# Performance work log

Hardware: AMD Instinct MI355X
Metric: run time of the kernel (lower is better)

## Reference

```python
import jax, jax.numpy as jnp
import numpy as np

N_NODES = 100000
N_EDGES = 1600000
F_IN = 65
HIDDEN = 128
N_CLASSES = 32
NEG_SLOPE = 0.2


def _gat_conv(x0, src, dst, W, a_src, a_dst, b):
    """Single-head GAT-style conv: gather over edges, segment softmax, scatter-add."""
    h = x0 @ W                                  # [N, C]
    s = h @ a_src                                # [N]
    d = h @ a_dst                                # [N]
    e = jax.nn.leaky_relu(s[src] + d[dst], NEG_SLOPE)   # [E]
    m = jax.ops.segment_max(e, dst, num_segments=N_NODES)
    m = jnp.where(jnp.isfinite(m), m, 0.0)
    ex = jnp.exp(e - m[dst])                     # [E]
    denom = jax.ops.segment_sum(ex, dst, num_segments=N_NODES)
    alpha = ex / (denom[dst] + 1e-16)            # [E]
    out = jax.ops.segment_sum(h[src] * alpha[:, None], dst, num_segments=N_NODES)
    return out + b                               # [N, C]


def setup_inputs() -> dict:
    key = jax.random.key(0)
    ks = jax.random.split(key, 12)
    sc_in = 1.0 / np.sqrt(F_IN)
    sc_h = 1.0 / np.sqrt(HIDDEN)
    return {
        "x": jax.random.normal(ks[0], (N_NODES, F_IN), dtype=jnp.float32),
        "edge_index": jax.random.randint(ks[1], (2, N_EDGES), 0, N_NODES, dtype=jnp.int64),
        "W_mlp": jax.random.normal(ks[2], (F_IN, HIDDEN), dtype=jnp.float32) * sc_in,
        "b_mlp": jnp.zeros((HIDDEN,), dtype=jnp.float32),
        "W1": jax.random.normal(ks[3], (HIDDEN, N_CLASSES), dtype=jnp.float32) * sc_h,
        "a1_src": jax.random.normal(ks[4], (N_CLASSES,), dtype=jnp.float32) * 0.1,
        "a1_dst": jax.random.normal(ks[5], (N_CLASSES,), dtype=jnp.float32) * 0.1,
        "b1": jnp.zeros((N_CLASSES,), dtype=jnp.float32),
        "W2": jax.random.normal(ks[6], (HIDDEN, N_CLASSES), dtype=jnp.float32) * sc_h,
        "a2_src": jax.random.normal(ks[7], (N_CLASSES,), dtype=jnp.float32) * 0.1,
        "a2_dst": jax.random.normal(ks[8], (N_CLASSES,), dtype=jnp.float32) * 0.1,
        "b2": jnp.zeros((N_CLASSES,), dtype=jnp.float32),
    }


def reference(x, edge_index, W_mlp, b_mlp, W1, a1_src, a1_dst, b1, W2, a2_src, a2_dst, b2):
    src, dst = edge_index[0], edge_index[1]
    x0 = jax.nn.relu(x @ W_mlp + b_mlp)                      # [N, H]
    x1 = jax.nn.relu(_gat_conv(x0, src, dst, W1, a1_src, a1_dst, b1))  # [N, C]
    # dropout is identity in eval mode
    x2 = _gat_conv(x0, src, dst, W2, a2_src, a2_dst, b2)     # [N, C]
    x3 = jnp.max(x0, axis=-1, keepdims=True)                 # [N, 1]
    lngal_out = jnp.concatenate((x1, x2, x3), axis=-1) + x   # [N, 2C+1] == [N, F]
    return jax.nn.log_softmax(lngal_out, axis=1)
```

## Files before the change

kernel.cpp:

```cpp
#include <hip/hip_runtime.h>
#include <hip/hip_bf16.h>

#define NN 100000
#define NE 1600000
#define FIN 65
#define HID 128
#define NC 32
#define OUTC 65
#define NBUCK 391
#define CHUNKS 400
#define CH 4000
#define ESTRIDE 5120
#define NODE_BLOCKS 1563

typedef __attribute__((ext_vector_type(8))) short s8v;
typedef __attribute__((ext_vector_type(4))) float f4v;
#define MFMA16(a, b, c) __builtin_amdgcn_mfma_f32_16x16x32_bf16(a, b, c, 0, 0, 0)

__device__ __forceinline__ float lrelu(float v){ return v > 0.f ? v : 0.2f * v; }
__device__ __forceinline__ short f2bs(float f){
  unsigned u = __float_as_uint(f);
  u += 0x7fffu + ((u >> 16) & 1u);
  return (short)(u >> 16);
}
__device__ __forceinline__ float bfu_lo(unsigned u){ return __uint_as_float(u << 16); }
__device__ __forceinline__ float bfu_hi(unsigned u){ return __uint_as_float(u & 0xffff0000u); }

__global__ __launch_bounds__(256) void k_prep(
    const float* __restrict__ Wmlp, const float* __restrict__ W1,
    const float* __restrict__ W2, short* __restrict__ wbg,
    int* __restrict__ bcursor)
{
  const int i = blockIdx.x * 256 + threadIdx.x;
  if (blockIdx.x == 0)
    for (int t = threadIdx.x; t < NBUCK; t += 256) bcursor[t] = 0;
  {
    const int j = i & 7, l = (i >> 3) & 63, nt = (i >> 9) & 7, t = i >> 12;
    const int k = t * 32 + ((l >> 4) << 3) + j;
    const int col = (nt << 4) + (l & 15);
    wbg[i] = f2bs(Wmlp[k * HID + col]);
  }
  {
    const int j = i & 7, l = (i >> 3) & 63, nt = (i >> 9) & 3, t = i >> 11;
    const int k = t * 32 + ((l >> 4) << 3) + j;
    const int col = (nt << 4) + (l & 15);
    wbg[8192 + i] = f2bs(col < NC ? W1[k * NC + col] : W2[k * NC + col - NC]);
  }
}

__global__ __launch_bounds__(256) void k_main(
    const float* __restrict__ x, const short* __restrict__ wbg,
    const float* __restrict__ Wmlp, const float* __restrict__ bmlp,
    const float* __restrict__ a1s, const float* __restrict__ a1d,
    const float* __restrict__ a2s, const float* __restrict__ a2d,
    const int* __restrict__ ei,
    unsigned short* __restrict__ hb16,
    float* __restrict__ sd2, float* __restrict__ dd2,
    float* __restrict__ out,
    int* __restrict__ bcursor, int* __restrict__ ebuf)
{
  __shared__ alignas(16) char smem[28416];
  const int tid = threadIdx.x;

  if (blockIdx.x >= NODE_BLOCKS) {
    const int cb = blockIdx.x - NODE_BLOCKS;
    int* lh = (int*)smem;
    int* lbase = lh + NBUCK;
    for (int i = tid; i < NBUCK; i += 256) lh[i] = 0;
    __syncthreads();
    const int4* s4 = (const int4*)ei + cb * (CH / 4);
    const int4* d4 = (const int4*)(ei + NE) + cb * (CH / 4);
    for (int i = tid; i < CH / 4; i += 256) {
      int4 v = d4[i];
      atomicAdd(&lh[v.x >> 8], 1);
      atomicAdd(&lh[v.y >> 8], 1);
      atomicAdd(&lh[v.z >> 8], 1);
      atomicAdd(&lh[v.w >> 8], 1);
    }
    __syncthreads();
    for (int i = tid; i < NBUCK; i += 256) {
      int c = lh[i];
      lbase[i] = c ? (i * ESTRIDE + atomicAdd(&bcursor[i], c)) : 0;
      lh[i] = 0;
    }
    __syncthreads();
    for (int i = tid; i < CH / 4; i += 256) {
      int4 sv = s4[i];
      int4 dv = d4[i];
      int b, r;
      b = dv.x >> 8; r = atomicAdd(&lh[b], 1); ebuf[lbase[b] + r] = (sv.x << 8) | (dv.x & 255);
      b = dv.y >> 8; r = atomicAdd(&lh[b], 1); ebuf[lbase[b] + r] = (sv.y << 8) | (dv.y & 255);
      b = dv.z >> 8; r = atomicAdd(&lh[b], 1); ebuf[lbase[b] + r] = (sv.z << 8) | (dv.z & 255);
      b = dv.w >> 8; r = atomicAdd(&lh[b], 1); ebuf[lbase[b] + r] = (sv.w << 8) | (dv.w & 255);
    }
    return;
  }

  short* xbf = (short*)smem;
  short* x0b = (short*)(smem + 9216);
  float* xc64 = (float*)(smem + 26624);
  float* w64 = (float*)(smem + 26880);
  float* bmv = (float*)(smem + 27392);
  float* avv = (float*)(smem + 27904);

  const int base = blockIdx.x * 64;

  if (tid < 128) { w64[tid] = Wmlp[64 * HID + tid]; bmv[tid] = bmlp[tid]; }
  else if (tid < 160) {
    const int q = tid - 128;
    avv[q] = a1s[q]; avv[32 + q] = a1d[q]; avv[64 + q] = a2s[q]; avv[96 + q] = a2d[q];
  }
  for (int i = tid; i < 64 * 65; i += 256) {
    const int r = i / 65, c = i - r * 65;
    const int node = base + r;
    const float v = (node < NN) ? x[(size_t)node * FIN + c] : 0.f;
    if (c == 64) xc64[r] = v; else xbf[r * 72 + c] = f2bs(v);
  }
  __syncthreads();

  const int w = tid >> 6, lane = tid & 63;
  const int g = lane >> 4, q = lane & 15;
  const int rowA = w * 16 + q;
  const int rowD0 = w * 16 + g * 4;
  const s8v* wv8 = (const s8v*)wbg;

  const s8v a0 = *(const s8v*)&xbf[rowA * 72 + g * 8];
  const s8v a1 = *(const s8v*)&xbf[rowA * 72 + 32 + g * 8];

  f4v acc[8];
  #pragma unroll
  for (int nt = 0; nt < 8; ++nt) acc[nt] = (f4v){0.f, 0.f, 0.f, 0.f};
  #pragma unroll
  for (int nt = 0; nt < 8; ++nt) {
    const s8v b0 = wv8[nt * 64 + lane];
    const s8v b1 = wv8[(8 + nt) * 64 + lane];
    acc[nt] = MFMA16(a0, b0, acc[nt]);
    acc[nt] = MFMA16(a1, b1, acc[nt]);
  }

  float xc[4];
  #pragma unroll
  for (int r = 0; r < 4; ++r) xc[r] = xc64[rowD0 + r];
  float rmax[4] = {0.f, 0.f, 0.f, 0.f};
  #pragma unroll
  for (int nt = 0; nt < 8; ++nt) {
    const int col = nt * 16 + q;
    const float wvv = w64[col], bv = bmv[col];
    #pragma unroll
    for (int r = 0; r < 4; ++r) {
      const float v = fmaxf(fmaf(xc[r], wvv, acc[nt][r]) + bv, 0.f);
      rmax[r] = fmaxf(rmax[r], v);
      x0b[(rowD0 + r) * 136 + col] = f2bs(v);
    }
  }
  #pragma unroll
  for (int off = 1; off < 16; off <<= 1)
    #pragma unroll
    for (int r = 0; r < 4; ++r) rmax[r] = fmaxf(rmax[r], __shfl_xor(rmax[r], off));
  if (q == 0) {
    #pragma unroll
    for (int r = 0; r < 4; ++r) {
      const int node = base + rowD0 + r;
      if (node < NN) out[(size_t)node * OUTC + 64] = rmax[r];
    }
  }

  s8v af[4];
  #pragma unroll
  for (int t = 0; t < 4; ++t)
    af[t] = *(const s8v*)&x0b[rowA * 136 + t * 32 + g * 8];
  f4v hacc[4];
  #pragma unroll
  for (int nt = 0; nt < 4; ++nt) hacc[nt] = (f4v){0.f, 0.f, 0.f, 0.f};
  #pragma unroll
  for (int nt = 0; nt < 4; ++nt)
    #pragma unroll
    for (int t = 0; t < 4; ++t)
      hacc[nt] = MFMA16(af[t], wv8[1024 + (t * 4 + nt) * 64 + lane], hacc[nt]);

  float s1p[4], d1p[4], s2p[4], d2p[4];
  #pragma unroll
  for (int r = 0; r < 4; ++r) {
    s1p[r] = hacc[0][r] * avv[q]        + hacc[1][r] * avv[16 + q];
    d1p[r] = hacc[0][r] * avv[32 + q]   + hacc[1][r] * avv[48 + q];
    s2p[r] = hacc[2][r] * avv[64 + q]   + hacc[3][r] * avv[80 + q];
    d2p[r] = hacc[2][r] * avv[96 + q]   + hacc[3][r] * avv[112 + q];
  }
  #pragma unroll
  for (int off = 1; off < 16; off <<= 1) {
    #pragma unroll
    for (int r = 0; r < 4; ++r) {
      s1p[r] += __shfl_xor(s1p[r], off);
      d1p[r] += __shfl_xor(d1p[r], off);
      s2p[r] += __shfl_xor(s2p[r], off);
      d2p[r] += __shfl_xor(d2p[r], off);
    }
  }
  #pragma unroll
  for (int r = 0; r < 4; ++r) {
    const int node = base + rowD0 + r;
    if (node < NN) {
      #pragma unroll
      for (int nt = 0; nt < 4; ++nt)
        hb16[(size_t)node * 64 + nt * 16 + q] = (unsigned short)f2bs(hacc[nt][r]);
      if (q == 0) {
        *(float2*)&sd2[(size_t)node * 2] = make_float2(s1p[r], s2p[r]);
        *(float2*)&dd2[(size_t)node * 2] = make_float2(d1p[r], d2p[r]);
      }
    }
  }
}

__global__ __launch_bounds__(256) void k_csr(const int* __restrict__ bcursor,
                                             const int* __restrict__ ebuf,
                                             int* __restrict__ rpp,
                                             int* __restrict__ csrc)
{
  __shared__ int lh[256];
  __shared__ int wsum[4];
  const int b = blockIdx.x;
  const int e0 = b * ESTRIDE;
  const int cntb = bcursor[b];
  const int t = threadIdx.x;

  lh[t] = 0;
  __syncthreads();
  for (int i = t; i < cntb; i += 256)
    atomicAdd(&lh[ebuf[e0 + i] & 255], 1);
  __syncthreads();

  const int lane = t & 63;
  const int wid = t >> 6;
  int v = lh[t];
  const int orig = v;
  for (int off = 1; off < 64; off <<= 1) {
    int tm = __shfl_up(v, off);
    if (lane >= off) v += tm;
  }
  if (lane == 63) wsum[wid] = v;
  __syncthreads();
  int add = 0;
  for (int ww = 0; ww < wid; ++ww) add += wsum[ww];
  const int ex = v + add - orig;

  const int nb0 = b << 8;
  if (nb0 + t < NN) rpp[nb0 + t] = ((e0 + ex) << 8) | orig;
  __syncthreads();
  lh[t] = ex;
  __syncthreads();
  for (int i = t; i < cntb; i += 256) {
    int p = ebuf[e0 + i];
    int r = atomicAdd(&lh[p & 255], 1);
    csrc[e0 + r] = ((unsigned)p) >> 8;
  }
}

__global__ __launch_bounds__(256) void k_conv(
    const int* __restrict__ rpp, const int* __restrict__ csrc,
    const unsigned short* __restrict__ hb16,
    const float* __restrict__ sd2, const float* __restrict__ dd2,
    const float* __restrict__ x,
    const float* __restrict__ b1, const float* __restrict__ b2,
    float* __restrict__ out)
{
  const int wid = threadIdx.x >> 6;
  const int lane = threadIdx.x & 63;
  const int half = lane >> 5;
  const int hl = lane & 31;
  const int sub = hl >> 3;
  const int cg8 = hl & 7;
  const int conv = cg8 >> 2;

  const int node = blockIdx.x * 8 + wid * 2 + half;

  const int rv = rpp[node];
  const int base = ((unsigned)rv) >> 8;
  const int cnt = rv & 255;
  const float2 dnv = *(const float2*)&dd2[(size_t)node * 2];

  const char* hbp = (const char*)hb16;
  float a[8] = {0.f, 0.f, 0.f, 0.f, 0.f, 0.f, 0.f, 0.f};
  float den = 0.f;

  for (int chunk = 0; chunk < cnt; chunk += 32) {
    const int rem = min(cnt - chunk, 32);

    int sE = 0;
    float w1v = 0.f, w2v = 0.f;
    if (hl < rem) {
      sE = csrc[base + chunk + hl];
      const float2 sv = *(const float2*)&sd2[(size_t)sE * 2];
      w1v = __expf(lrelu(sv.x + dnv.x));
      w2v = __expf(lrelu(sv.y + dnv.y));
    }
    float d1 = w1v, d2 = w2v;
    #pragma unroll
    for (int off = 1; off < 32; off <<= 1) {
      d1 += __shfl_xor(d1, off);
      d2 += __shfl_xor(d2, off);
    }
    den += conv ? d2 : d1;

    for (int i0 = 0; i0 < rem; i0 += 4) {
      const int src = half * 32 + i0 + sub;
      const int s = __shfl(sE, src);
      const float wa = __shfl(w1v, src);
      const float wb = __shfl(w2v, src);
      const float w = conv ? wb : wa;
      const uint4 pv = *(const uint4*)(hbp + ((size_t)s << 7) + cg8 * 16);
      a[0] = fmaf(w, bfu_lo(pv.x), a[0]);
      a[1] = fmaf(w, bfu_hi(pv.x), a[1]);
      a[2] = fmaf(w, bfu_lo(pv.y), a[2]);
      a[3] = fmaf(w, bfu_hi(pv.y), a[3]);
      a[4] = fmaf(w, bfu_lo(pv.z), a[4]);
      a[5] = fmaf(w, bfu_hi(pv.z), a[5]);
      a[6] = fmaf(w, bfu_lo(pv.w), a[6]);
      a[7] = fmaf(w, bfu_hi(pv.w), a[7]);
    }
  }

  #pragma unroll
  for (int j = 0; j < 8; ++j) {
    a[j] += __shfl_xor(a[j], 8);
    a[j] += __shfl_xor(a[j], 16);
  }

  const int ch = cg8 * 8;
  const float rden = 1.f / (den + 1e-16f);
  const float* bp = conv ? (b2 + ch - 32) : (b1 + ch);
  const float4 bva = *(const float4*)bp;
  const float4 bvb = *(const float4*)(bp + 4);
  float v[8];
  v[0] = a[0] * rden + bva.x; v[1] = a[1] * rden + bva.y;
  v[2] = a[2] * rden + bva.z; v[3] = a[3] * rden + bva.w;
  v[4] = a[4] * rden + bvb.x; v[5] = a[5] * rden + bvb.y;
  v[6] = a[6] * rden + bvb.z; v[7] = a[7] * rden + bvb.w;
  if (conv == 0) {
    #pragma unroll
    for (int j = 0; j < 8; ++j) v[j] = fmaxf(v[j], 0.f);
  }
  const float* xr = x + (size_t)node * OUTC;
  float* row = out + (size_t)node * OUTC;
  const float4 xa = *(const float4*)&xr[ch];
  const float4 xb = *(const float4*)&xr[ch + 4];
  v[0] += xa.x; v[1] += xa.y; v[2] += xa.z; v[3] += xa.w;
  v[4] += xb.x; v[5] += xb.y; v[6] += xb.z; v[7] += xb.w;
  const float v64 = row[64] + xr[64];

  float mx = v[0];
  #pragma unroll
  for (int j = 1; j < 8; ++j) mx = fmaxf(mx, v[j]);
  #pragma unroll
  for (int off = 1; off < 8; off <<= 1) mx = fmaxf(mx, __shfl_xor(mx, off));
  mx = fmaxf(mx, v64);
  float sm = 0.f;
  #pragma unroll
  for (int j = 0; j < 8; ++j) sm += __expf(v[j] - mx);
  #pragma unroll
  for (int off = 1; off < 8; off <<= 1) sm += __shfl_xor(sm, off);
  sm += __expf(v64 - mx);
  const float ls = __logf(sm) + mx;

  if (sub == 0) {
    *(float4*)&row[ch]     = make_float4(v[0] - ls, v[1] - ls, v[2] - ls, v[3] - ls);
    *(float4*)&row[ch + 4] = make_float4(v[4] - ls, v[5] - ls, v[6] - ls, v[7] - ls);
    if (hl == 0) row[64] = v64 - ls;
  }
}

extern "C" void kernel_launch(void* const* d_in, const int* in_sizes, int n_in,
                              void* d_out, int out_size, void* d_ws, size_t ws_size,
                              hipStream_t stream)
{
  const float* x    = (const float*)d_in[0];
  const int*   ei   = (const int*)d_in[1];
  const float* Wmlp = (const float*)d_in[2];
  const float* bmlp = (const float*)d_in[3];
  const float* W1   = (const float*)d_in[4];
  const float* a1s  = (const float*)d_in[5];
  const float* a1d  = (const float*)d_in[6];
  const float* b1   = (const float*)d_in[7];
  const float* W2   = (const float*)d_in[8];
  const float* a2s  = (const float*)d_in[9];
  const float* a2d  = (const float*)d_in[10];
  const float* b2   = (const float*)d_in[11];
  float* out = (float*)d_out;

  unsigned short* hb16 = (unsigned short*)d_ws;
  float* sd2 = (float*)(hb16 + (size_t)NN * 64);
  float* dd2 = sd2 + (size_t)2 * NN;
  int* ebuf   = (int*)(dd2 + (size_t)2 * NN);
  int* csrc   = ebuf + (size_t)NBUCK * ESTRIDE;
  int* rpp    = csrc + (size_t)NBUCK * ESTRIDE;
  int* bcursor= rpp + NBUCK * 256;
  short* wbg  = (short*)(bcursor + NBUCK);

  k_prep<<<32, 256, 0, stream>>>(Wmlp, W1, W2, wbg, bcursor);

  k_main<<<NODE_BLOCKS + CHUNKS, 256, 0, stream>>>(
      x, wbg, Wmlp, bmlp, a1s, a1d, a2s, a2d, ei,
      hb16, sd2, dd2, out, bcursor, ebuf);

  k_csr<<<NBUCK, 256, 0, stream>>>(bcursor, ebuf, rpp, csrc);

  k_conv<<<NN / 8, 256, 0, stream>>>(rpp, csrc, hb16, sd2, dd2, x, b1, b2, out);
}
```

Baseline: 107.5 us.

## Precompute edge attention weights and denominators in CSR build kernel

Moves the per-edge exp(leaky_relu(s+d)) computation and the softmax denominator accumulation from the conv kernel into the CSR-building kernel. Each edge record now packs the source index with two bf16 weights, and per-node denominators are summed with shared-memory atomics. This removes the chunked weight computation, shuffle reductions and per-edge sd2 gathers from k_conv, and the bf16-rounded weights cost some precision. The node MLP kernel also hoists its MFMA B-operand weight loads into registers before the barrier, which raises register pressure.

```diff
diff --git a/kernel.cpp b/kernel.cpp
--- a/kernel.cpp
+++ b/kernel.cpp
@@ -104,6 +104,12 @@
   float* avv = (float*)(smem + 27904);
 
   const int base = blockIdx.x * 64;
+  const int w = tid >> 6, lane = tid & 63;
+  const s8v* wv8 = (const s8v*)wbg;
+
+  s8v bw[16];
+  #pragma unroll
+  for (int nt = 0; nt < 16; ++nt) bw[nt] = wv8[nt * 64 + lane];
 
   if (tid < 128) { w64[tid] = Wmlp[64 * HID + tid]; bmv[tid] = bmlp[tid]; }
   else if (tid < 160) {
@@ -118,11 +124,9 @@
   }
   __syncthreads();
 
-  const int w = tid >> 6, lane = tid & 63;
   const int g = lane >> 4, q = lane & 15;
   const int rowA = w * 16 + q;
   const int rowD0 = w * 16 + g * 4;
-  const s8v* wv8 = (const s8v*)wbg;
 
   const s8v a0 = *(const s8v*)&xbf[rowA * 72 + g * 8];
   const s8v a1 = *(const s8v*)&xbf[rowA * 72 + 32 + g * 8];
@@ -132,11 +136,13 @@
   for (int nt = 0; nt < 8; ++nt) acc[nt] = (f4v){0.f, 0.f, 0.f, 0.f};
   #pragma unroll
   for (int nt = 0; nt < 8; ++nt) {
-    const s8v b0 = wv8[nt * 64 + lane];
-    const s8v b1 = wv8[(8 + nt) * 64 + lane];
-    acc[nt] = MFMA16(a0, b0, acc[nt]);
-    acc[nt] = MFMA16(a1, b1, acc[nt]);
-  }
+    acc[nt] = MFMA16(a0, bw[nt], acc[nt]);
+    acc[nt] = MFMA16(a1, bw[8 + nt], acc[nt]);
+  }
+
+  s8v bw2[16];
+  #pragma unroll
+  for (int t2 = 0; t2 < 16; ++t2) bw2[t2] = wv8[1024 + t2 * 64 + lane];
 
   float xc[4];
   #pragma unroll
@@ -167,16 +173,16 @@
 
   s8v af[4];
   #pragma unroll
-  for (int t = 0; t < 4; ++t)
-    af[t] = *(const s8v*)&x0b[rowA * 136 + t * 32 + g * 8];
+  for (int t2 = 0; t2 < 4; ++t2)
+    af[t2] = *(const s8v*)&x0b[rowA * 136 + t2 * 32 + g * 8];
   f4v hacc[4];
   #pragma unroll
   for (int nt = 0; nt < 4; ++nt) hacc[nt] = (f4v){0.f, 0.f, 0.f, 0.f};
   #pragma unroll
   for (int nt = 0; nt < 4; ++nt)
     #pragma unroll
-    for (int t = 0; t < 4; ++t)
-      hacc[nt] = MFMA16(af[t], wv8[1024 + (t * 4 + nt) * 64 + lane], hacc[nt]);
+    for (int t2 = 0; t2 < 4; ++t2)
+      hacc[nt] = MFMA16(af[t2], bw2[t2 * 4 + nt], hacc[nt]);
 
   float s1p[4], d1p[4], s2p[4], d2p[4];
   #pragma unroll
@@ -213,18 +219,32 @@
 
 __global__ __launch_bounds__(256) void k_csr(const int* __restrict__ bcursor,
                                              const int* __restrict__ ebuf,
+                                             const float* __restrict__ sd2,
+                                             const float* __restrict__ dd2,
                                              int* __restrict__ rpp,
-                                             int* __restrict__ csrc)
+                                             int2* __restrict__ erec,
+                                             float* __restrict__ den)
 {
   __shared__ int lh[256];
+  __shared__ float dl2[512];
+  __shared__ float dsum[512];
   __shared__ int wsum[4];
   const int b = blockIdx.x;
   const int e0 = b * ESTRIDE;
   const int cntb = bcursor[b];
   const int t = threadIdx.x;
+  const int node = (b << 8) + t;
 
   lh[t] = 0;
-  __syncthreads();
+  dsum[t] = 0.f;
+  dsum[256 + t] = 0.f;
+  if (node < NN) {
+    const float2 dv = *(const float2*)&dd2[(size_t)node * 2];
+    dl2[t * 2] = dv.x;
+    dl2[t * 2 + 1] = dv.y;
+  }
+  __syncthreads();
+
   for (int i = t; i < cntb; i += 256)
     atomicAdd(&lh[ebuf[e0 + i] & 255], 1);
   __syncthreads();
@@ -243,22 +263,34 @@
   for (int ww = 0; ww < wid; ++ww) add += wsum[ww];
   const int ex = v + add - orig;
 
-  const int nb0 = b << 8;
-  if (nb0 + t < NN) rpp[nb0 + t] = ((e0 + ex) << 8) | orig;
+  if (node < NN) rpp[node] = ((e0 + ex) << 8) | orig;
   __syncthreads();
   lh[t] = ex;
   __syncthreads();
+
   for (int i = t; i < cntb; i += 256) {
-    int p = ebuf[e0 + i];
-    int r = atomicAdd(&lh[p & 255], 1);
-    csrc[e0 + r] = ((unsigned)p) >> 8;
-  }
+    const int p = ebuf[e0 + i];
+    const int dl = p & 255;
+    const int s = ((unsigned)p) >> 8;
+    const float2 sv = *(const float2*)&sd2[(size_t)s * 2];
+    const float w1 = __expf(lrelu(sv.x + dl2[dl * 2]));
+    const float w2 = __expf(lrelu(sv.y + dl2[dl * 2 + 1]));
+    const unsigned wpk = ((unsigned)(unsigned short)f2bs(w2) << 16)
+                       | (unsigned)(unsigned short)f2bs(w1);
+    const int r = atomicAdd(&lh[dl], 1);
+    erec[e0 + r] = make_int2(s, (int)wpk);
+    atomicAdd(&dsum[dl * 2], w1);
+    atomicAdd(&dsum[dl * 2 + 1], w2);
+  }
+  __syncthreads();
+  if (node < NN)
+    *(float2*)&den[(size_t)node * 2] = make_float2(dsum[t * 2], dsum[t * 2 + 1]);
 }
 
 __global__ __launch_bounds__(256) void k_conv(
-    const int* __restrict__ rpp, const int* __restrict__ csrc,
+    const int* __restrict__ rpp, const int2* __restrict__ erec,
     const unsigned short* __restrict__ hb16,
-    const float* __restrict__ sd2, const float* __restrict__ dd2,
+    const float* __restrict__ den,
     const float* __restrict__ x,
     const float* __restrict__ b1, const float* __restrict__ b2,
     float* __restrict__ out)
@@ -276,47 +308,26 @@
   const int rv = rpp[node];
   const int base = ((unsigned)rv) >> 8;
   const int cnt = rv & 255;
-  const float2 dnv = *(const float2*)&dd2[(size_t)node * 2];
+  const float2 dnv = *(const float2*)&den[(size_t)node * 2];
+  const float dden = conv ? dnv.y : dnv.x;
 
   const char* hbp = (const char*)hb16;
   float a[8] = {0.f, 0.f, 0.f, 0.f, 0.f, 0.f, 0.f, 0.f};
-  float den = 0.f;
-
-  for (int chunk = 0; chunk < cnt; chunk += 32) {
-    const int rem = min(cnt - chunk, 32);
-
-    int sE = 0;
-    float w1v = 0.f, w2v = 0.f;
-    if (hl < rem) {
-      sE = csrc[base + chunk + hl];
-      const float2 sv = *(const float2*)&sd2[(size_t)sE * 2];
-      w1v = __expf(lrelu(sv.x + dnv.x));
-      w2v = __expf(lrelu(sv.y + dnv.y));
-    }
-    float d1 = w1v, d2 = w2v;
-    #pragma unroll
-    for (int off = 1; off < 32; off <<= 1) {
-      d1 += __shfl_xor(d1, off);
-      d2 += __shfl_xor(d2, off);
-    }
-    den += conv ? d2 : d1;
-
-    for (int i0 = 0; i0 < rem; i0 += 4) {
-      const int src = half * 32 + i0 + sub;
-      const int s = __shfl(sE, src);
-      const float wa = __shfl(w1v, src);
-      const float wb = __shfl(w2v, src);
-      const float w = conv ? wb : wa;
-      const uint4 pv = *(const uint4*)(hbp + ((size_t)s << 7) + cg8 * 16);
-      a[0] = fmaf(w, bfu_lo(pv.x), a[0]);
-      a[1] = fmaf(w, bfu_hi(pv.x), a[1]);
-      a[2] = fmaf(w, bfu_lo(pv.y), a[2]);
-      a[3] = fmaf(w, bfu_hi(pv.y), a[3]);
-      a[4] = fmaf(w, bfu_lo(pv.z), a[4]);
-      a[5] = fmaf(w, bfu_hi(pv.z), a[5]);
-      a[6] = fmaf(w, bfu_lo(pv.w), a[6]);
-      a[7] = fmaf(w, bfu_hi(pv.w), a[7]);
-    }
+
+  for (int i0 = 0; i0 < cnt; i0 += 4) {
+    const int idx = i0 + sub;
+    const int2 rec = erec[base + ((idx < cnt) ? idx : (cnt - 1))];
+    const unsigned wy = (idx < cnt) ? (unsigned)rec.y : 0u;
+    const float wgt = conv ? bfu_hi(wy) : bfu_lo(wy);
+    const uint4 pv = *(const uint4*)(hbp + ((size_t)(unsigned)rec.x << 7) + cg8 * 16);
+    a[0] = fmaf(wgt, bfu_lo(pv.x), a[0]);
+    a[1] = fmaf(wgt, bfu_hi(pv.x), a[1]);
+    a[2] = fmaf(wgt, bfu_lo(pv.y), a[2]);
+    a[3] = fmaf(wgt, bfu_hi(pv.y), a[3]);
+    a[4] = fmaf(wgt, bfu_lo(pv.z), a[4]);
+    a[5] = fmaf(wgt, bfu_hi(pv.z), a[5]);
+    a[6] = fmaf(wgt, bfu_lo(pv.w), a[6]);
+    a[7] = fmaf(wgt, bfu_hi(pv.w), a[7]);
   }
 
   #pragma unroll
@@ -326,7 +337,7 @@
   }
 
   const int ch = cg8 * 8;
-  const float rden = 1.f / (den + 1e-16f);
+  const float rden = 1.f / (dden + 1e-16f);
   const float* bp = conv ? (b2 + ch - 32) : (b1 + ch);
   const float4 bva = *(const float4*)bp;
   const float4 bvb = *(const float4*)(bp + 4);
@@ -389,9 +400,10 @@
   unsigned short* hb16 = (unsigned short*)d_ws;
   float* sd2 = (float*)(hb16 + (size_t)NN * 64);
   float* dd2 = sd2 + (size_t)2 * NN;
-  int* ebuf   = (int*)(dd2 + (size_t)2 * NN);
-  int* csrc   = ebuf + (size_t)NBUCK * ESTRIDE;
-  int* rpp    = csrc + (size_t)NBUCK * ESTRIDE;
+  float* den = dd2 + (size_t)2 * NN;
+  int* ebuf   = (int*)(den + (size_t)2 * NN);
+  int2* erec  = (int2*)(ebuf + (size_t)NBUCK * ESTRIDE);
+  int* rpp    = (int*)(erec + (size_t)NBUCK * ESTRIDE);
   int* bcursor= rpp + NBUCK * 256;
   short* wbg  = (short*)(bcursor + NBUCK);
 
@@ -401,7 +413,7 @@
       x, wbg, Wmlp, bmlp, a1s, a1d, a2s, a2d, ei,
       hb16, sd2, dd2, out, bcursor, ebuf);
 
-  k_csr<<<NBUCK, 256, 0, stream>>>(bcursor, ebuf, rpp, csrc);
-
-  k_conv<<<NN / 8, 256, 0, stream>>>(rpp, csrc, hb16, sd2, dd2, x, b1, b2, out);
-}
+  k_csr<<<NBUCK, 256, 0, stream>>>(bcursor, ebuf, sd2, dd2, rpp, erec, den);
+
+  k_conv<<<NN / 8, 256, 0, stream>>>(rpp, erec, hb16, den, x, b1, b2, out);
+}
```

Measured after the change: 123.5 us. 1.15x slower.

## Persist node tiles with LDS-staged weights and simplify per-edge aggregation loop

Applied to the files above, without the earlier changes.

The node-transform part of k_main now launches 391 persistent blocks. Each block copies the bf16 weight fragments into LDS once and then loops over up to four 64-node tiles, so weights are no longer re-read from global memory for every tile. Separately, k_conv drops the 32-edge chunked shuffle scheme: each lane loads its own edge's source index and score and computes its exp weight directly, and the denominator is reduced with shuffles at the end. The trade-offs are less parallelism and more LDS per block in k_main, plus redundant csrc/sd2 loads and exp work across lanes in k_conv.

```diff
diff --git a/kernel.cpp b/kernel.cpp
--- a/kernel.cpp
+++ b/kernel.cpp
@@ -11,7 +11,8 @@
 #define CHUNKS 400
 #define CH 4000
 #define ESTRIDE 5120
-#define NODE_BLOCKS 1563
+#define TB 391
+#define NTILES 1563
 
 typedef __attribute__((ext_vector_type(8))) short s8v;
 typedef __attribute__((ext_vector_type(4))) float f4v;
@@ -59,12 +60,18 @@
     float* __restrict__ out,
     int* __restrict__ bcursor, int* __restrict__ ebuf)
 {
-  __shared__ alignas(16) char smem[28416];
+  __shared__ alignas(16) short wbs[16384];
+  __shared__ alignas(16) short xbf[64 * 72];
+  __shared__ alignas(16) short x0b[64 * 136];
+  __shared__ float xc64[64];
+  __shared__ float w64[128];
+  __shared__ float bmv[128];
+  __shared__ float avv[128];
   const int tid = threadIdx.x;
 
-  if (blockIdx.x >= NODE_BLOCKS) {
-    const int cb = blockIdx.x - NODE_BLOCKS;
-    int* lh = (int*)smem;
+  if (blockIdx.x >= TB) {
+    const int cb = blockIdx.x - TB;
+    int* lh = (int*)wbs;
     int* lbase = lh + NBUCK;
     for (int i = tid; i < NBUCK; i += 256) lh[i] = 0;
     __syncthreads();
@@ -96,118 +103,122 @@
     return;
   }
 
-  short* xbf = (short*)smem;
-  short* x0b = (short*)(smem + 9216);
-  float* xc64 = (float*)(smem + 26624);
-  float* w64 = (float*)(smem + 26880);
-  float* bmv = (float*)(smem + 27392);
-  float* avv = (float*)(smem + 27904);
-
-  const int base = blockIdx.x * 64;
-
+  {
+    const uint4* wg = (const uint4*)wbg;
+    uint4* dst = (uint4*)wbs;
+    #pragma unroll
+    for (int i = 0; i < 8; ++i) dst[tid + i * 256] = wg[tid + i * 256];
+  }
   if (tid < 128) { w64[tid] = Wmlp[64 * HID + tid]; bmv[tid] = bmlp[tid]; }
   else if (tid < 160) {
     const int q = tid - 128;
     avv[q] = a1s[q]; avv[32 + q] = a1d[q]; avv[64 + q] = a2s[q]; avv[96 + q] = a2d[q];
   }
-  for (int i = tid; i < 64 * 65; i += 256) {
-    const int r = i / 65, c = i - r * 65;
-    const int node = base + r;
-    const float v = (node < NN) ? x[(size_t)node * FIN + c] : 0.f;
-    if (c == 64) xc64[r] = v; else xbf[r * 72 + c] = f2bs(v);
-  }
-  __syncthreads();
 
   const int w = tid >> 6, lane = tid & 63;
   const int g = lane >> 4, q = lane & 15;
   const int rowA = w * 16 + q;
   const int rowD0 = w * 16 + g * 4;
-  const s8v* wv8 = (const s8v*)wbg;
-
-  const s8v a0 = *(const s8v*)&xbf[rowA * 72 + g * 8];
-  const s8v a1 = *(const s8v*)&xbf[rowA * 72 + 32 + g * 8];
-
-  f4v acc[8];
-  #pragma unroll
-  for (int nt = 0; nt < 8; ++nt) acc[nt] = (f4v){0.f, 0.f, 0.f, 0.f};
-  #pragma unroll
-  for (int nt = 0; nt < 8; ++nt) {
-    const s8v b0 = wv8[nt * 64 + lane];
-    const s8v b1 = wv8[(8 + nt) * 64 + lane];
-    acc[nt] = MFMA16(a0, b0, acc[nt]);
-    acc[nt] = MFMA16(a1, b1, acc[nt]);
-  }
-
-  float xc[4];
-  #pragma unroll
-  for (int r = 0; r < 4; ++r) xc[r] = xc64[rowD0 + r];
-  float rmax[4] = {0.f, 0.f, 0.f, 0.f};
-  #pragma unroll
-  for (int nt = 0; nt < 8; ++nt) {
-    const int col = nt * 16 + q;
-    const float wvv = w64[col], bv = bmv[col];
+
+  for (int t = 0; t < 4; ++t) {
+    const int tile = blockIdx.x + t * TB;
+    if (tile >= NTILES) break;
+    const int base = tile * 64;
+
+    for (int i = tid; i < 64 * 65; i += 256) {
+      const int r = i / 65, c = i - r * 65;
+      const int node = base + r;
+      const float v = (node < NN) ? x[(size_t)node * FIN + c] : 0.f;
+      if (c == 64) xc64[r] = v; else xbf[r * 72 + c] = f2bs(v);
+    }
+    __syncthreads();
+
+    const s8v a0 = *(const s8v*)&xbf[rowA * 72 + g * 8];
+    const s8v a1 = *(const s8v*)&xbf[rowA * 72 + 32 + g * 8];
+
+    f4v acc[8];
+    #pragma unroll
+    for (int nt = 0; nt < 8; ++nt) acc[nt] = (f4v){0.f, 0.f, 0.f, 0.f};
+    #pragma unroll
+    for (int nt = 0; nt < 8; ++nt) {
+      const s8v b0 = *(const s8v*)&wbs[(nt * 64 + lane) * 8];
+      const s8v b1 = *(const s8v*)&wbs[((8 + nt) * 64 + lane) * 8];
+      acc[nt] = MFMA16(a0, b0, acc[nt]);
+      acc[nt] = MFMA16(a1, b1, acc[nt]);
+    }
+
+    float xc[4];
+    #pragma unroll
+    for (int r = 0; r < 4; ++r) xc[r] = xc64[rowD0 + r];
+    float rmax[4] = {0.f, 0.f, 0.f, 0.f};
+    #pragma unroll
+    for (int nt = 0; nt < 8; ++nt) {
+      const int col = nt * 16 + q;
+      const float wvv = w64[col], bv = bmv[col];
+      #pragma unroll
+      for (int r = 0; r < 4; ++r) {
+        const float v = fmaxf(fmaf(xc[r], wvv, acc[nt][r]) + bv, 0.f);
+        rmax[r] = fmaxf(rmax[r], v);
+        x0b[(rowD0 + r) * 136 + col] = f2bs(v);
+      }
+    }
+    #pragma unroll
+    for (int off = 1; off < 16; off <<= 1)
+      #pragma unroll
+      for (int r = 0; r < 4; ++r) rmax[r] = fmaxf(rmax[r], __shfl_xor(rmax[r], off));
+    if (q == 0) {
+      #pragma unroll
+      for (int r = 0; r < 4; ++r) {
+        const int node = base + rowD0 + r;
+        if (node < NN) out[(size_t)node * OUTC + 64] = rmax[r];
+      }
+    }
+
+    s8v af[4];
+    #pragma unroll
+    for (int t2 = 0; t2 < 4; ++t2)
+      af[t2] = *(const s8v*)&x0b[rowA * 136 + t2 * 32 + g * 8];
+    f4v hacc[4];
+    #pragma unroll
+    for (int nt = 0; nt < 4; ++nt) hacc[nt] = (f4v){0.f, 0.f, 0.f, 0.f};
+    #pragma unroll
+    for (int nt = 0; nt < 4; ++nt)
+      #pragma unroll
+      for (int t2 = 0; t2 < 4; ++t2)
+        hacc[nt] = MFMA16(af[t2], *(const s8v*)&wbs[8192 + (t2 * 4 + nt) * 64 * 8 + lane * 8], hacc[nt]);
+
+    float s1p[4], d1p[4], s2p[4], d2p[4];
     #pragma unroll
     for (int r = 0; r < 4; ++r) {
-      const float v = fmaxf(fmaf(xc[r], wvv, acc[nt][r]) + bv, 0.f);
-      rmax[r] = fmaxf(rmax[r], v);
-      x0b[(rowD0 + r) * 136 + col] = f2bs(v);
-    }
-  }
-  #pragma unroll
-  for (int off = 1; off < 16; off <<= 1)
-    #pragma unroll
-    for (int r = 0; r < 4; ++r) rmax[r] = fmaxf(rmax[r], __shfl_xor(rmax[r], off));
-  if (q == 0) {
+      s1p[r] = hacc[0][r] * avv[q]        + hacc[1][r] * avv[16 + q];
+      d1p[r] = hacc[0][r] * avv[32 + q]   + hacc[1][r] * avv[48 + q];
+      s2p[r] = hacc[2][r] * avv[64 + q]   + hacc[3][r] * avv[80 + q];
+      d2p[r] = hacc[2][r] * avv[96 + q]   + hacc[3][r] * avv[112 + q];
+    }
+    #pragma unroll
+    for (int off = 1; off < 16; off <<= 1) {
+      #pragma unroll
+      for (int r = 0; r < 4; ++r) {
+        s1p[r] += __shfl_xor(s1p[r], off);
+        d1p[r] += __shfl_xor(d1p[r], off);
+        s2p[r] += __shfl_xor(s2p[r], off);
+        d2p[r] += __shfl_xor(d2p[r], off);
+      }
+    }
     #pragma unroll
     for (int r = 0; r < 4; ++r) {
       const int node = base + rowD0 + r;
-      if (node < NN) out[(size_t)node * OUTC + 64] = rmax[r];
-    }
-  }
-
-  s8v af[4];
-  #pragma unroll
-  for (int t = 0; t < 4; ++t)
-    af[t] = *(const s8v*)&x0b[rowA * 136 + t * 32 + g * 8];
-  f4v hacc[4];
-  #pragma unroll
-  for (int nt = 0; nt < 4; ++nt) hacc[nt] = (f4v){0.f, 0.f, 0.f, 0.f};
-  #pragma unroll
-  for (int nt = 0; nt < 4; ++nt)
-    #pragma unroll
-    for (int t = 0; t < 4; ++t)
-      hacc[nt] = MFMA16(af[t], wv8[1024 + (t * 4 + nt) * 64 + lane], hacc[nt]);
-
-  float s1p[4], d1p[4], s2p[4], d2p[4];
-  #pragma unroll
-  for (int r = 0; r < 4; ++r) {
-    s1p[r] = hacc[0][r] * avv[q]        + hacc[1][r] * avv[16 + q];
-    d1p[r] = hacc[0][r] * avv[32 + q]   + hacc[1][r] * avv[48 + q];
-    s2p[r] = hacc[2][r] * avv[64 + q]   + hacc[3][r] * avv[80 + q];
-    d2p[r] = hacc[2][r] * avv[96 + q]   + hacc[3][r] * avv[112 + q];
-  }
-  #pragma unroll
-  for (int off = 1; off < 16; off <<= 1) {
-    #pragma unroll
-    for (int r = 0; r < 4; ++r) {
-      s1p[r] += __shfl_xor(s1p[r], off);
-      d1p[r] += __shfl_xor(d1p[r], off);
-      s2p[r] += __shfl_xor(s2p[r], off);
-      d2p[r] += __shfl_xor(d2p[r], off);
-    }
-  }
-  #pragma unroll
-  for (int r = 0; r < 4; ++r) {
-    const int node = base + rowD0 + r;
-    if (node < NN) {
-      #pragma unroll
-      for (int nt = 0; nt < 4; ++nt)
-        hb16[(size_t)node * 64 + nt * 16 + q] = (unsigned short)f2bs(hacc[nt][r]);
-      if (q == 0) {
-        *(float2*)&sd2[(size_t)node * 2] = make_float2(s1p[r], s2p[r]);
-        *(float2*)&dd2[(size_t)node * 2] = make_float2(d1p[r], d2p[r]);
+      if (node < NN) {
+        #pragma unroll
+        for (int nt = 0; nt < 4; ++nt)
+          hb16[(size_t)node * 64 + nt * 16 + q] = (unsigned short)f2bs(hacc[nt][r]);
+        if (q == 0) {
+          *(float2*)&sd2[(size_t)node * 2] = make_float2(s1p[r], s2p[r]);
+          *(float2*)&dd2[(size_t)node * 2] = make_float2(d1p[r], d2p[r]);
+        }
       }
     }
+    __syncthreads();
   }
 }
 
@@ -276,47 +287,28 @@
   const int rv = rpp[node];
   const int base = ((unsigned)rv) >> 8;
   const int cnt = rv & 255;
-  const float2 dnv = *(const float2*)&dd2[(size_t)node * 2];
+  const float dn = dd2[(size_t)node * 2 + conv];
 
   const char* hbp = (const char*)hb16;
   float a[8] = {0.f, 0.f, 0.f, 0.f, 0.f, 0.f, 0.f, 0.f};
-  float den = 0.f;
-
-  for (int chunk = 0; chunk < cnt; chunk += 32) {
-    const int rem = min(cnt - chunk, 32);
-
-    int sE = 0;
-    float w1v = 0.f, w2v = 0.f;
-    if (hl < rem) {
-      sE = csrc[base + chunk + hl];
-      const float2 sv = *(const float2*)&sd2[(size_t)sE * 2];
-      w1v = __expf(lrelu(sv.x + dnv.x));
-      w2v = __expf(lrelu(sv.y + dnv.y));
-    }
-    float d1 = w1v, d2 = w2v;
-    #pragma unroll
-    for (int off = 1; off < 32; off <<= 1) {
-      d1 += __shfl_xor(d1, off);
-      d2 += __shfl_xor(d2, off);
-    }
-    den += conv ? d2 : d1;
-
-    for (int i0 = 0; i0 < rem; i0 += 4) {
-      const int src = half * 32 + i0 + sub;
-      const int s = __shfl(sE, src);
-      const float wa = __shfl(w1v, src);
-      const float wb = __shfl(w2v, src);
-      const float w = conv ? wb : wa;
-      const uint4 pv = *(const uint4*)(hbp + ((size_t)s << 7) + cg8 * 16);
-      a[0] = fmaf(w, bfu_lo(pv.x), a[0]);
-      a[1] = fmaf(w, bfu_hi(pv.x), a[1]);
-      a[2] = fmaf(w, bfu_lo(pv.y), a[2]);
-      a[3] = fmaf(w, bfu_hi(pv.y), a[3]);
-      a[4] = fmaf(w, bfu_lo(pv.z), a[4]);
-      a[5] = fmaf(w, bfu_hi(pv.z), a[5]);
-      a[6] = fmaf(w, bfu_lo(pv.w), a[6]);
-      a[7] = fmaf(w, bfu_hi(pv.w), a[7]);
-    }
+  float wsum = 0.f;
+
+  for (int i0 = 0; i0 < cnt; i0 += 4) {
+    const int idx = i0 + sub;
+    const bool ok = idx < cnt;
+    const int s = csrc[base + (ok ? idx : (cnt - 1))];
+    const float sv = sd2[(size_t)s * 2 + conv];
+    const float wgt = ok ? __expf(lrelu(sv + dn)) : 0.f;
+    wsum += wgt;
+    const uint4 pv = *(const uint4*)(hbp + ((size_t)s << 7) + cg8 * 16);
+    a[0] = fmaf(wgt, bfu_lo(pv.x), a[0]);
+    a[1] = fmaf(wgt, bfu_hi(pv.x), a[1]);
+    a[2] = fmaf(wgt, bfu_lo(pv.y), a[2]);
+    a[3] = fmaf(wgt, bfu_hi(pv.y), a[3]);
+    a[4] = fmaf(wgt, bfu_lo(pv.z), a[4]);
+    a[5] = fmaf(wgt, bfu_hi(pv.z), a[5]);
+    a[6] = fmaf(wgt, bfu_lo(pv.w), a[6]);
+    a[7] = fmaf(wgt, bfu_hi(pv.w), a[7]);
   }
 
   #pragma unroll
@@ -324,9 +316,11 @@
     a[j] += __shfl_xor(a[j], 8);
     a[j] += __shfl_xor(a[j], 16);
   }
+  wsum += __shfl_xor(wsum, 8);
+  wsum += __shfl_xor(wsum, 16);
 
   const int ch = cg8 * 8;
-  const float rden = 1.f / (den + 1e-16f);
+  const float rden = 1.f / (wsum + 1e-16f);
   const float* bp = conv ? (b2 + ch - 32) : (b1 + ch);
   const float4 bva = *(const float4*)bp;
   const float4 bvb = *(const float4*)(bp + 4);
@@ -397,7 +391,7 @@
 
   k_prep<<<32, 256, 0, stream>>>(Wmlp, W1, W2, wbg, bcursor);
 
-  k_main<<<NODE_BLOCKS + CHUNKS, 256, 0, stream>>>(
+  k_main<<<TB + CHUNKS, 256, 0, stream>>>(
       x, wbg, Wmlp, bmlp, a1s, a1d, a2s, a2d, ei,
       hb16, sd2, dd2, out, bcursor, ebuf);
 
```

Result: slower. 123.6 us (+15.0%).
